# Kernel optimization log

Hardware: AMD Instinct MI355X
Metric: run time of the kernel (lower is better)

## Reference

```python
import jax, jax.numpy as jnp
import numpy as np

IN_FEATURES = 4096
OUT_FEATURES = 8192
GROUP_SIZE = 16
NUM_GROUPS = IN_FEATURES * OUT_FEATURES // GROUP_SIZE  # 2_097_152


def block_dequantize_2bit(packed, normalization):
    # packed: [G, group_size//4] int32 holding uint8 values; norm: [G, 1] fp16
    shifts = jnp.arange(4, dtype=packed.dtype) * 2  # bit offsets 0,2,4,6
    # unpacked column 4k+i comes from packed column k, bits 2i..2i+1
    u = ((packed[:, :, None] >> shifts) & 3).astype(jnp.float32)  # [G, gs/4, 4]
    u = u.reshape(packed.shape[0], -1)  # [G, group_size]
    norm = normalization.astype(jnp.float32)
    return (u / 3.0) * (2.0 * norm) - norm  # [G, group_size]


def setup_inputs() -> dict:
    key = jax.random.key(0)
    k_x, k_q, k_n, k_b = jax.random.split(key, 4)
    x = jax.random.normal(k_x, (256, IN_FEATURES), dtype=jnp.float32)
    # packed 2-bit weights: random bytes (store as int32 for clean bit ops in jax)
    weight_q2 = jax.random.randint(k_q, (NUM_GROUPS, GROUP_SIZE // 4), 0, 256, dtype=jnp.int32)
    # per-group normalization (abs-max), positive, fp16 as in the module buffer
    weight_norm = (jax.random.uniform(k_n, (NUM_GROUPS, 1), dtype=jnp.float32) * 0.05 + 1e-4).astype(jnp.float16)
    bias = jax.random.normal(k_b, (OUT_FEATURES,), dtype=jnp.float32) * 0.01
    return {"x": x, "weight_q2": weight_q2, "weight_norm": weight_norm, "bias": bias}


def reference(x, weight_q2, weight_norm, bias):
    weight = block_dequantize_2bit(weight_q2, weight_norm).reshape(OUT_FEATURES, IN_FEATURES)
    return jnp.dot(x.astype(jnp.float32), weight.T) + bias
```

## Files before the change

### kernel.cpp

```cpp
#include <hip/hip_runtime.h>
#include <hip/hip_bf16.h>
#include <hip/hip_fp16.h>

#define IN_F   4096
#define OUT_F  8192
#define M_ROWS 256

#define SPLITK 4
#define K_SPL  (IN_F / SPLITK)
#define NIT    (K_SPL / 64)

typedef __attribute__((ext_vector_type(8))) short  short8;
typedef __attribute__((ext_vector_type(4))) float  float4v;

__device__ inline unsigned int pack_bf16(float lo, float hi) {
    return __builtin_amdgcn_perm(__float_as_uint(hi), __float_as_uint(lo), 0x07060302u);
}

__device__ inline int sw_idx(int row, int kchunk) {
    return row * 64 + ((kchunk ^ (row & 7)) << 3);
}

__global__ void cvt_x_kernel(const float* __restrict__ x, unsigned short* __restrict__ xb) {
    int i = blockIdx.x * blockDim.x + threadIdx.x;
    if (i < (M_ROWS * IN_F) / 4) {
        float4 v = ((const float4*)x)[i];
        uint2 o;
        o.x = pack_bf16(v.x, v.y);
        o.y = pack_bf16(v.z, v.w);
        ((uint2*)xb)[i] = o;
    }
}

__global__ void init_out_kernel(const float* __restrict__ bias, float* __restrict__ out) {
    int i = blockIdx.x * blockDim.x + threadIdx.x;
    if (i < (M_ROWS * OUT_F) / 4) {
        float4 b = ((const float4*)bias)[i & (OUT_F / 4 - 1)];
        ((float4*)out)[i] = b;
    }
}

__device__ inline void load_a16_f32(const float* __restrict__ p, uint4& o0, uint4& o1) {
    float4 v0 = ((const float4*)p)[0], v1 = ((const float4*)p)[1];
    float4 v2 = ((const float4*)p)[2], v3 = ((const float4*)p)[3];
    o0.x = pack_bf16(v0.x, v0.y); o0.y = pack_bf16(v0.z, v0.w);
    o0.z = pack_bf16(v1.x, v1.y); o0.w = pack_bf16(v1.z, v1.w);
    o1.x = pack_bf16(v2.x, v2.y); o1.y = pack_bf16(v2.z, v2.w);
    o1.z = pack_bf16(v3.x, v3.y); o1.w = pack_bf16(v3.z, v3.w);
}

template <bool XB>
__global__ __launch_bounds__(256, 4) void gemm2bit_kernel(
    const float*           __restrict__ xf,
    const unsigned short*  __restrict__ xb,
    const int*             __restrict__ wq,
    const void*            __restrict__ wnorm,
    float*                 __restrict__ out)
{
    __shared__ unsigned short lds[2][2][64 * 64];

    const int t    = threadIdx.x;
    const int n0   = blockIdx.x * 64;
    const int m0   = blockIdx.y * 64;
    const int kb   = blockIdx.z * K_SPL;
    const int wave = t >> 6;
    const int lane = t & 63;
    const int l15  = lane & 15;
    const int quad = lane >> 4;
    const int wm   = (wave >> 1) * 32;
    const int wn   = (wave & 1) * 32;

    const float cand0 = *(const float*)wnorm;
    const bool  nf32  = (cand0 > 1e-5f && cand0 < 0.1f);

    const int srow = t >> 2;
    const int skc  = t & 3;
    const int c0   = skc * 2;
    const int wO0  = sw_idx(srow, c0);
    const int wO1  = sw_idx(srow, c0 + 1);

    int fa0[2], fa1[2], fb0[2], fb1[2];
#pragma unroll
    for (int kk = 0; kk < 2; ++kk) {
        fa0[kk] = sw_idx(wm +      l15, kk * 4 + quad);
        fa1[kk] = sw_idx(wm + 16 + l15, kk * 4 + quad);
        fb0[kk] = sw_idx(wn +      l15, kk * 4 + quad);
        fb1[kk] = sw_idx(wn + 16 + l15, kk * 4 + quad);
    }

    const int arow = m0 + srow;
    const int brow = n0 + srow;
    const float*          nrmF = (const float*)wnorm;
    const __half*         nrmH = (const __half*)wnorm;

    float4v acc[2][2] = {};

    uint4 aN0, aN1; int4 qN; float nN;
    {
        if (XB) {
            const unsigned short* p = xb + arow * IN_F + kb + skc * 16;
            aN0 = *(const uint4*)p;
            aN1 = *(const uint4*)(p + 8);
        } else {
            load_a16_f32(xf + arow * IN_F + kb + skc * 16, aN0, aN1);
        }
        qN = *(const int4*)(wq + brow * (IN_F / 4) + (kb >> 2) + skc * 4);
        const int gi = brow * (IN_F / 16) + (kb >> 4) + skc;
        nN = nf32 ? nrmF[gi] : __half2float(nrmH[gi]);
    }

    for (int ito = 0; ito < NIT / 2; ++ito) {
#pragma unroll
        for (int half = 0; half < 2; ++half) {
            const int it = ito * 2 + half;

            uint4 aC0 = aN0, aC1 = aN1;
            int4  qC  = qN;
            float nC  = nN;

            if (it < NIT - 1) {
                const int kn = kb + ((it + 1) << 6);
                if (XB) {
                    const unsigned short* p = xb + arow * IN_F + kn + skc * 16;
                    aN0 = *(const uint4*)p;
                    aN1 = *(const uint4*)(p + 8);
                } else {
                    load_a16_f32(xf + arow * IN_F + kn + skc * 16, aN0, aN1);
                }
                qN = *(const int4*)(wq + brow * (IN_F / 4) + (kn >> 2) + skc * 4);
                const int gi = brow * (IN_F / 16) + (kn >> 4) + skc;
                nN = nf32 ? nrmF[gi] : __half2float(nrmH[gi]);
            }

            const float s = nC * (2.0f / 3.0f);
            float f[16];
            const int qa[4] = {qC.x, qC.y, qC.z, qC.w};
#pragma unroll
            for (int bq = 0; bq < 4; ++bq) {
#pragma unroll
                for (int i = 0; i < 4; ++i)
                    f[bq * 4 + i] = fmaf((float)((qa[bq] >> (2 * i)) & 3), s, -nC);
            }
            uint4 bv0, bv1;
            bv0.x = pack_bf16(f[0],  f[1]);   bv0.y = pack_bf16(f[2],  f[3]);
            bv0.z = pack_bf16(f[4],  f[5]);   bv0.w = pack_bf16(f[6],  f[7]);
            bv1.x = pack_bf16(f[8],  f[9]);   bv1.y = pack_bf16(f[10], f[11]);
            bv1.z = pack_bf16(f[12], f[13]);  bv1.w = pack_bf16(f[14], f[15]);

            unsigned short* LA = lds[half][0];
            unsigned short* LB = lds[half][1];
            *(uint4*)&LA[wO0] = aC0;
            *(uint4*)&LA[wO1] = aC1;
            *(uint4*)&LB[wO0] = bv0;
            *(uint4*)&LB[wO1] = bv1;

            __syncthreads();

#pragma unroll
            for (int kk = 0; kk < 2; ++kk) {
                short8 a0 = *(const short8*)&LA[fa0[kk]];
                short8 a1 = *(const short8*)&LA[fa1[kk]];
                short8 b0 = *(const short8*)&LB[fb0[kk]];
                short8 b1 = *(const short8*)&LB[fb1[kk]];
                acc[0][0] = __builtin_amdgcn_mfma_f32_16x16x32_bf16(a0, b0, acc[0][0], 0, 0, 0);
                acc[0][1] = __builtin_amdgcn_mfma_f32_16x16x32_bf16(a0, b1, acc[0][1], 0, 0, 0);
                acc[1][0] = __builtin_amdgcn_mfma_f32_16x16x32_bf16(a1, b0, acc[1][0], 0, 0, 0);
                acc[1][1] = __builtin_amdgcn_mfma_f32_16x16x32_bf16(a1, b1, acc[1][1], 0, 0, 0);
            }
        }
    }

#pragma unroll
    for (int j = 0; j < 2; ++j) {
        const int col = n0 + wn + j * 16 + l15;
#pragma unroll
        for (int i = 0; i < 2; ++i) {
            const int row0 = m0 + wm + i * 16 + quad * 4;
#pragma unroll
            for (int r = 0; r < 4; ++r) {
                atomicAdd(&out[(row0 + r) * OUT_F + col], acc[i][j][r]);
            }
        }
    }
}

extern "C" void kernel_launch(void* const* d_in, const int* in_sizes, int n_in,
                              void* d_out, int out_size, void* d_ws, size_t ws_size,
                              hipStream_t stream) {
    const float*          x    = (const float*)d_in[0];
    const int*            wq   = (const int*)d_in[1];
    const void*           wn   = (const void*)d_in[2];
    const float*          bias = (const float*)d_in[3];
    float*                out  = (float*)d_out;

    const bool use_ws = ws_size >= (size_t)(M_ROWS * IN_F * sizeof(unsigned short));

    dim3 grid(OUT_F / 64, M_ROWS / 64, SPLITK);

    init_out_kernel<<<dim3((M_ROWS * OUT_F / 4) / 256), 256, 0, stream>>>(bias, out);

    if (use_ws) {
        unsigned short* xb = (unsigned short*)d_ws;
        cvt_x_kernel<<<dim3((M_ROWS * IN_F / 4 + 255) / 256), 256, 0, stream>>>(x, xb);
        gemm2bit_kernel<true><<<grid, 256, 0, stream>>>(nullptr, xb, wq, wn, out);
    } else {
        gemm2bit_kernel<false><<<grid, 256, 0, stream>>>(x, nullptr, wq, wn, out);
    }
}
```

Baseline: 133.2 us.

## Drop LDS staging; load MFMA fragments directly with pre-swizzled activations

The GEMM no longer stages tiles through shared memory. Activations are converted once into a bf16 layout that already matches the MFMA fragment order, so each lane reads its operand with one coalesced 16-byte load. Each wave now owns a 64x64 output tile and dequantizes its own weight fragments in registers, with two k-steps kept in flight for prefetch, which removes the LDS writes, reads and barriers. In exchange, each wave carries 16 accumulators and holds more registers, the launch bound drops to one block per SM hint, and activation loads are repeated by the four waves of a block instead of being shared.

New measurement: 169.6 us. 1.27x slower.

```diff
diff --git a/kernel.cpp b/kernel.cpp
--- a/kernel.cpp
+++ b/kernel.cpp
@@ -1,5 +1,4 @@
 #include <hip/hip_runtime.h>
-#include <hip/hip_bf16.h>
 #include <hip/hip_fp16.h>
 
 #define IN_F   4096
@@ -8,28 +7,32 @@
 
 #define SPLITK 4
 #define K_SPL  (IN_F / SPLITK)
-#define NIT    (K_SPL / 64)
+#define NIT    (K_SPL / 32)
+#define KS_TOT (IN_F / 32)
 
 typedef __attribute__((ext_vector_type(8))) short  short8;
 typedef __attribute__((ext_vector_type(4))) float  float4v;
+
+union pk8 { uint4 u; short8 s; };
 
 __device__ inline unsigned int pack_bf16(float lo, float hi) {
     return __builtin_amdgcn_perm(__float_as_uint(hi), __float_as_uint(lo), 0x07060302u);
 }
 
-__device__ inline int sw_idx(int row, int kchunk) {
-    return row * 64 + ((kchunk ^ (row & 7)) << 3);
-}
-
-__global__ void cvt_x_kernel(const float* __restrict__ x, unsigned short* __restrict__ xb) {
-    int i = blockIdx.x * blockDim.x + threadIdx.x;
-    if (i < (M_ROWS * IN_F) / 4) {
-        float4 v = ((const float4*)x)[i];
-        uint2 o;
-        o.x = pack_bf16(v.x, v.y);
-        o.y = pack_bf16(v.z, v.w);
-        ((uint2*)xb)[i] = o;
-    }
+__global__ void cvt_x_kernel(const float* __restrict__ x, uint4* __restrict__ xb) {
+    const int tid = blockIdx.x * blockDim.x + threadIdx.x;
+    if (tid >= (M_ROWS * IN_F) / 8) return;
+    const int lane = tid & 63;
+    const int mf   = (tid >> 6) & 15;
+    const int ks   = tid >> 10;
+    const int m    = mf * 16 + (lane & 15);
+    const int k    = ks * 32 + (lane >> 4) * 8;
+    const float* p = x + m * IN_F + k;
+    float4 v0 = ((const float4*)p)[0], v1 = ((const float4*)p)[1];
+    uint4 o;
+    o.x = pack_bf16(v0.x, v0.y); o.y = pack_bf16(v0.z, v0.w);
+    o.z = pack_bf16(v1.x, v1.y); o.w = pack_bf16(v1.z, v1.w);
+    xb[tid] = o;
 }
 
 __global__ void init_out_kernel(const float* __restrict__ bias, float* __restrict__ out) {
@@ -40,146 +43,113 @@
     }
 }
 
-__device__ inline void load_a16_f32(const float* __restrict__ p, uint4& o0, uint4& o1) {
-    float4 v0 = ((const float4*)p)[0], v1 = ((const float4*)p)[1];
-    float4 v2 = ((const float4*)p)[2], v3 = ((const float4*)p)[3];
-    o0.x = pack_bf16(v0.x, v0.y); o0.y = pack_bf16(v0.z, v0.w);
-    o0.z = pack_bf16(v1.x, v1.y); o0.w = pack_bf16(v1.z, v1.w);
-    o1.x = pack_bf16(v2.x, v2.y); o1.y = pack_bf16(v2.z, v2.w);
-    o1.z = pack_bf16(v3.x, v3.y); o1.w = pack_bf16(v3.z, v3.w);
-}
-
 template <bool XB>
-__global__ __launch_bounds__(256, 4) void gemm2bit_kernel(
-    const float*           __restrict__ xf,
-    const unsigned short*  __restrict__ xb,
-    const int*             __restrict__ wq,
-    const void*            __restrict__ wnorm,
-    float*                 __restrict__ out)
+__global__ __launch_bounds__(256, 1) void gemm2bit_kernel(
+    const float* __restrict__ xf,
+    const uint4* __restrict__ xb,
+    const int*   __restrict__ wq,
+    const void*  __restrict__ wnorm,
+    float*       __restrict__ out)
 {
-    __shared__ unsigned short lds[2][2][64 * 64];
-
     const int t    = threadIdx.x;
-    const int n0   = blockIdx.x * 64;
-    const int m0   = blockIdx.y * 64;
-    const int kb   = blockIdx.z * K_SPL;
     const int wave = t >> 6;
     const int lane = t & 63;
     const int l15  = lane & 15;
     const int quad = lane >> 4;
-    const int wm   = (wave >> 1) * 32;
-    const int wn   = (wave & 1) * 32;
+
+    const int nb   = blockIdx.x * 256 + wave * 64;
+    const int m0   = blockIdx.y * 64;
+    const int mb   = blockIdx.y * 4;
+    const int ks0  = blockIdx.z * NIT;
 
     const float cand0 = *(const float*)wnorm;
     const bool  nf32  = (cand0 > 1e-5f && cand0 < 0.1f);
 
-    const int srow = t >> 2;
-    const int skc  = t & 3;
-    const int c0   = skc * 2;
-    const int wO0  = sw_idx(srow, c0);
-    const int wO1  = sw_idx(srow, c0 + 1);
+    const char* wqB = (const char*)wq;
+    const char* nmB = (const char*)wnorm;
 
-    int fa0[2], fa1[2], fb0[2], fb1[2];
+    int qOff[4], nOff[4];
 #pragma unroll
-    for (int kk = 0; kk < 2; ++kk) {
-        fa0[kk] = sw_idx(wm +      l15, kk * 4 + quad);
-        fa1[kk] = sw_idx(wm + 16 + l15, kk * 4 + quad);
-        fb0[kk] = sw_idx(wn +      l15, kk * 4 + quad);
-        fb1[kk] = sw_idx(wn + 16 + l15, kk * 4 + quad);
+    for (int j = 0; j < 4; ++j) {
+        const int n = nb + j * 16 + l15;
+        qOff[j] = n * (IN_F / 4) * 4 + quad * 8;
+        nOff[j] = nf32 ? (n * (IN_F / 16) * 4 + (quad >> 1) * 4)
+                       : (n * (IN_F / 16) * 2 + (quad >> 1) * 2);
     }
 
-    const int arow = m0 + srow;
-    const int brow = n0 + srow;
-    const float*          nrmF = (const float*)wnorm;
-    const __half*         nrmH = (const __half*)wnorm;
+    float4v acc[4][4] = {};
 
-    float4v acc[2][2] = {};
+    auto loadA = [&](uint4 (&a)[4], int ks) {
+        if (XB) {
+#pragma unroll
+            for (int i = 0; i < 4; ++i)
+                a[i] = xb[(ks * 16 + mb + i) * 64 + lane];
+        } else {
+#pragma unroll
+            for (int i = 0; i < 4; ++i) {
+                const float* p = xf + (m0 + i * 16 + l15) * IN_F + ks * 32 + quad * 8;
+                float4 v0 = ((const float4*)p)[0], v1 = ((const float4*)p)[1];
+                a[i].x = pack_bf16(v0.x, v0.y); a[i].y = pack_bf16(v0.z, v0.w);
+                a[i].z = pack_bf16(v1.x, v1.y); a[i].w = pack_bf16(v1.z, v1.w);
+            }
+        }
+    };
 
-    uint4 aN0, aN1; int4 qN; float nN;
-    {
-        if (XB) {
-            const unsigned short* p = xb + arow * IN_F + kb + skc * 16;
-            aN0 = *(const uint4*)p;
-            aN1 = *(const uint4*)(p + 8);
-        } else {
-            load_a16_f32(xf + arow * IN_F + kb + skc * 16, aN0, aN1);
+    auto loadB = [&](int2 (&q)[4], float (&nm)[4], int ks) {
+#pragma unroll
+        for (int j = 0; j < 4; ++j) {
+            q[j]  = *(const int2*)(wqB + qOff[j] + ks * 32);
+            nm[j] = nf32 ? *(const float*)(nmB + nOff[j] + ks * 8)
+                         : __half2float(*(const __half*)(nmB + nOff[j] + ks * 4));
         }
-        qN = *(const int4*)(wq + brow * (IN_F / 4) + (kb >> 2) + skc * 4);
-        const int gi = brow * (IN_F / 16) + (kb >> 4) + skc;
-        nN = nf32 ? nrmF[gi] : __half2float(nrmH[gi]);
-    }
+    };
+
+    auto process = [&](uint4 (&a)[4], int2 (&q)[4], float (&nm)[4]) {
+#pragma unroll
+        for (int j = 0; j < 4; ++j) {
+            const float nC = nm[j];
+            const float s  = nC * (2.0f / 3.0f);
+            const int q0 = q[j].x, q1 = q[j].y;
+            float f0 = fmaf((float)( q0       & 3), s, -nC);
+            float f1 = fmaf((float)((q0 >> 2) & 3), s, -nC);
+            float f2 = fmaf((float)((q0 >> 4) & 3), s, -nC);
+            float f3 = fmaf((float)((q0 >> 6) & 3), s, -nC);
+            float f4 = fmaf((float)( q1       & 3), s, -nC);
+            float f5 = fmaf((float)((q1 >> 2) & 3), s, -nC);
+            float f6 = fmaf((float)((q1 >> 4) & 3), s, -nC);
+            float f7 = fmaf((float)((q1 >> 6) & 3), s, -nC);
+            pk8 b;
+            b.u.x = pack_bf16(f0, f1); b.u.y = pack_bf16(f2, f3);
+            b.u.z = pack_bf16(f4, f5); b.u.w = pack_bf16(f6, f7);
+#pragma unroll
+            for (int i = 0; i < 4; ++i) {
+                pk8 av; av.u = a[i];
+                acc[i][j] = __builtin_amdgcn_mfma_f32_16x16x32_bf16(av.s, b.s, acc[i][j], 0, 0, 0);
+            }
+        }
+    };
+
+    uint4 a0[4], a1[4]; int2 q0v[4], q1v[4]; float n0v[4], n1v[4];
+    loadA(a0, ks0);     loadB(q0v, n0v, ks0);
+    loadA(a1, ks0 + 1); loadB(q1v, n1v, ks0 + 1);
 
     for (int ito = 0; ito < NIT / 2; ++ito) {
-#pragma unroll
-        for (int half = 0; half < 2; ++half) {
-            const int it = ito * 2 + half;
-
-            uint4 aC0 = aN0, aC1 = aN1;
-            int4  qC  = qN;
-            float nC  = nN;
-
-            if (it < NIT - 1) {
-                const int kn = kb + ((it + 1) << 6);
-                if (XB) {
-                    const unsigned short* p = xb + arow * IN_F + kn + skc * 16;
-                    aN0 = *(const uint4*)p;
-                    aN1 = *(const uint4*)(p + 8);
-                } else {
-                    load_a16_f32(xf + arow * IN_F + kn + skc * 16, aN0, aN1);
-                }
-                qN = *(const int4*)(wq + brow * (IN_F / 4) + (kn >> 2) + skc * 4);
-                const int gi = brow * (IN_F / 16) + (kn >> 4) + skc;
-                nN = nf32 ? nrmF[gi] : __half2float(nrmH[gi]);
-            }
-
-            const float s = nC * (2.0f / 3.0f);
-            float f[16];
-            const int qa[4] = {qC.x, qC.y, qC.z, qC.w};
-#pragma unroll
-            for (int bq = 0; bq < 4; ++bq) {
-#pragma unroll
-                for (int i = 0; i < 4; ++i)
-                    f[bq * 4 + i] = fmaf((float)((qa[bq] >> (2 * i)) & 3), s, -nC);
-            }
-            uint4 bv0, bv1;
-            bv0.x = pack_bf16(f[0],  f[1]);   bv0.y = pack_bf16(f[2],  f[3]);
-            bv0.z = pack_bf16(f[4],  f[5]);   bv0.w = pack_bf16(f[6],  f[7]);
-            bv1.x = pack_bf16(f[8],  f[9]);   bv1.y = pack_bf16(f[10], f[11]);
-            bv1.z = pack_bf16(f[12], f[13]);  bv1.w = pack_bf16(f[14], f[15]);
-
-            unsigned short* LA = lds[half][0];
-            unsigned short* LB = lds[half][1];
-            *(uint4*)&LA[wO0] = aC0;
-            *(uint4*)&LA[wO1] = aC1;
-            *(uint4*)&LB[wO0] = bv0;
-            *(uint4*)&LB[wO1] = bv1;
-
-            __syncthreads();
-
-#pragma unroll
-            for (int kk = 0; kk < 2; ++kk) {
-                short8 a0 = *(const short8*)&LA[fa0[kk]];
-                short8 a1 = *(const short8*)&LA[fa1[kk]];
-                short8 b0 = *(const short8*)&LB[fb0[kk]];
-                short8 b1 = *(const short8*)&LB[fb1[kk]];
-                acc[0][0] = __builtin_amdgcn_mfma_f32_16x16x32_bf16(a0, b0, acc[0][0], 0, 0, 0);
-                acc[0][1] = __builtin_amdgcn_mfma_f32_16x16x32_bf16(a0, b1, acc[0][1], 0, 0, 0);
-                acc[1][0] = __builtin_amdgcn_mfma_f32_16x16x32_bf16(a1, b0, acc[1][0], 0, 0, 0);
-                acc[1][1] = __builtin_amdgcn_mfma_f32_16x16x32_bf16(a1, b1, acc[1][1], 0, 0, 0);
-            }
-        }
+        const int it = ks0 + ito * 2;
+        process(a0, q0v, n0v);
+        if (ito + 1 < NIT / 2) { loadA(a0, it + 2); loadB(q0v, n0v, it + 2); }
+        process(a1, q1v, n1v);
+        if (ito + 1 < NIT / 2) { loadA(a1, it + 3); loadB(q1v, n1v, it + 3); }
     }
 
 #pragma unroll
-    for (int j = 0; j < 2; ++j) {
-        const int col = n0 + wn + j * 16 + l15;
+    for (int j = 0; j < 4; ++j) {
+        const int col = nb + j * 16 + l15;
 #pragma unroll
-        for (int i = 0; i < 2; ++i) {
-            const int row0 = m0 + wm + i * 16 + quad * 4;
+        for (int i = 0; i < 4; ++i) {
+            const int row0 = m0 + i * 16 + quad * 4;
 #pragma unroll
-            for (int r = 0; r < 4; ++r) {
+            for (int r = 0; r < 4; ++r)
                 atomicAdd(&out[(row0 + r) * OUT_F + col], acc[i][j][r]);
-            }
         }
     }
 }
@@ -187,22 +157,22 @@
 extern "C" void kernel_launch(void* const* d_in, const int* in_sizes, int n_in,
                               void* d_out, int out_size, void* d_ws, size_t ws_size,
                               hipStream_t stream) {
-    const float*          x    = (const float*)d_in[0];
-    const int*            wq   = (const int*)d_in[1];
-    const void*           wn   = (const void*)d_in[2];
-    const float*          bias = (const float*)d_in[3];
-    float*                out  = (float*)d_out;
+    const float* x    = (const float*)d_in[0];
+    const int*   wq   = (const int*)d_in[1];
+    const void*  wn   = (const void*)d_in[2];
+    const float* bias = (const float*)d_in[3];
+    float*       out  = (float*)d_out;
 
     const bool use_ws = ws_size >= (size_t)(M_ROWS * IN_F * sizeof(unsigned short));
 
-    dim3 grid(OUT_F / 64, M_ROWS / 64, SPLITK);
+    dim3 grid(OUT_F / 256, M_ROWS / 64, SPLITK);
 
     init_out_kernel<<<dim3((M_ROWS * OUT_F / 4) / 256), 256, 0, stream>>>(bias, out);
 
     if (use_ws) {
-        unsigned short* xb = (unsigned short*)d_ws;
-        cvt_x_kernel<<<dim3((M_ROWS * IN_F / 4 + 255) / 256), 256, 0, stream>>>(x, xb);
-        gemm2bit_kernel<true><<<grid, 256, 0, stream>>>(nullptr, xb, wq, wn, out);
+        uint4* xbv = (uint4*)d_ws;
+        cvt_x_kernel<<<dim3((M_ROWS * IN_F / 8) / 256), 256, 0, stream>>>(x, xbv);
+        gemm2bit_kernel<true><<<grid, 256, 0, stream>>>(nullptr, xbv, wq, wn, out);
     } else {
         gemm2bit_kernel<false><<<grid, 256, 0, stream>>>(x, nullptr, wq, wn, out);
     }
```
